# Optimization experiments

Hardware: AMD Instinct MI355X
Metric: run time of the kernel (lower is better)

The kernel has to match this reference:

```python
import jax, jax.numpy as jnp
import numpy as np

B, E, H, T = 32768, 64, 128, 12  # batch, embedding_dim, decoder_h_dim, pred_len


def setup_inputs() -> dict:
    key = jax.random.key(0)
    ks = jax.random.split(key, 13)
    f = lambda k, shape: jax.random.normal(k, shape, dtype=jnp.float32) * 0.05
    return {
        "last_pos": f(ks[0], (B, 2)),
        "last_pos_rel": f(ks[1], (B, 2)),
        "h0": f(ks[2], (1, B, H)),
        "c0": f(ks[3], (1, B, H)),
        "pred_ped_speed": jax.random.uniform(ks[4], (T, B, 1), dtype=jnp.float32),
        # spatial_embedding: Linear(3, E)
        "W_se": f(ks[5], (E, 3)),
        "b_se": f(ks[6], (E,)),
        # single-layer LSTM(E -> H), torch gate order [i, f, g, o]
        "W_ih": f(ks[7], (4 * H, E)),
        "W_hh": f(ks[8], (4 * H, H)),
        "b_ih": f(ks[9], (4 * H,)),
        "b_hh": f(ks[10], (4 * H,)),
        # hidden2pos: Linear(H, 2)
        "W_hp": f(ks[11], (2, H)),
        "b_hp": f(ks[12], (2,)),
    }


def reference(last_pos, last_pos_rel, h0, c0, pred_ped_speed,
              W_se, b_se, W_ih, W_hh, b_ih, b_hh, W_hp, b_hp):
    # train_or_test == 0 path: speed comes straight from pred_ped_speed
    Tlen = pred_ped_speed.shape[0]
    b_lstm = b_ih + b_hh
    # initial decoder input: embed concat([last_pos_rel, speed_0])  -> [B, E]
    x0 = jnp.concatenate([last_pos_rel, pred_ped_speed[0]], axis=1) @ W_se.T + b_se

    def step(carry, t):
        h, c, x, lp = carry  # h,c: [B,H]; x: [B,E]; lp: [B,2]
        gates = x @ W_ih.T + h @ W_hh.T + b_lstm           # [B, 4H]
        i, f_, g, o = jnp.split(gates, 4, axis=1)
        c = jax.nn.sigmoid(f_) * c + jax.nn.sigmoid(i) * jnp.tanh(g)
        h = jax.nn.sigmoid(o) * jnp.tanh(c)
        rel = h @ W_hp.T + b_hp                            # [B, 2]
        lp = rel + lp                                      # curr_pos -> last_pos
        # speed for next step; at final step torch keeps the previous speed
        spd = pred_ped_speed[jnp.minimum(t + 1, Tlen - 1)]
        x = jnp.concatenate([rel, spd], axis=1) @ W_se.T + b_se
        return (h, c, x, lp), rel

    (h, c, _, _), rels = jax.lax.scan(
        step, (h0[0], c0[0], x0, last_pos), jnp.arange(Tlen))
    # pred_traj_fake_rel: [T, B, 2]; final hidden state: [1, B, H]
    return rels, h[None]
```

## Files before the change

### kernel.cpp

```cpp
#include <hip/hip_runtime.h>

#define T_LEN 12
#define B_N   32768
#define H_N   128
#define BM    64

typedef __attribute__((ext_vector_type(8))) __bf16 bf16x8;
typedef __attribute__((ext_vector_type(8))) short  short8v;
typedef __attribute__((ext_vector_type(4))) float  f32x4;

__device__ __forceinline__ unsigned short f2bf(float f) {
  unsigned int u = __builtin_bit_cast(unsigned int, f);
  u += 0x7fffu + ((u >> 16) & 1u);
  return (unsigned short)(u >> 16);
}
__device__ __forceinline__ float sigm(float x) {
  return __builtin_amdgcn_rcpf(1.f + __builtin_amdgcn_exp2f(-1.4426950408889634f * x));
}
__device__ __forceinline__ float tanh_(float x) {
  return 1.f - 2.f * __builtin_amdgcn_rcpf(__builtin_amdgcn_exp2f(2.8853900817779268f * x) + 1.f);
}

__global__ void prep_kernel(const float* __restrict__ Wih, const float* __restrict__ Whh,
                            const float* __restrict__ bih, const float* __restrict__ bhh,
                            const float* __restrict__ Wse, const float* __restrict__ bse,
                            const float* __restrict__ Whp, const float* __restrict__ bhp,
                            unsigned short* __restrict__ WfReg, unsigned short* __restrict__ WfGO,
                            unsigned short* __restrict__ pBg, float* __restrict__ u,
                            float* __restrict__ w0, float* __restrict__ G) {
  int i = blockIdx.x * 256 + threadIdx.x;
  if (i < 65536) {
    int row = i >> 7, k = i & 127;
    float s = Whh[row * 128 + k];
    float wh0 = Whp[k], wh1 = Whp[128 + k];
    for (int e = 0; e < 64; ++e)
      s += Wih[row * 64 + e] * (Wse[e * 3 + 0] * wh0 + Wse[e * 3 + 1] * wh1);
    unsigned short v = f2bf(s);
    int g = row >> 7, unit = row & 127, w = unit >> 4, l15 = unit & 15;
    int ks = k >> 5, kg = (k >> 3) & 3, j = k & 7, l = kg * 16 + l15;
    if (g < 2) WfReg[((g * 4 + ks) * 512 + w * 64 + l) * 8 + j] = v;
    else       WfGO[(((g - 2) * 4 + ks) * 512 + w * 64 + l) * 8 + j] = v;
  } else if (i < 65536 + 2048) {
    int j = i - 65536;
    int n = j >> 2, which = j & 3;
    float s = 0.f;
    if (which < 2) {
      for (int e = 0; e < 64; ++e) s += Wih[n * 64 + e] * Wse[e * 3 + which];
      G[n * 2 + which] = s;
    } else if (which == 2) {
      for (int e = 0; e < 64; ++e) s += Wih[n * 64 + e] * Wse[e * 3 + 2];
      u[n] = s;
    } else {
      for (int e = 0; e < 64; ++e)
        s += Wih[n * 64 + e] * (bse[e] + Wse[e * 3 + 0] * bhp[0] + Wse[e * 3 + 1] * bhp[1]);
      w0[n] = bih[n] + bhh[n] + s;
    }
  } else if (i < 65536 + 2048 + 2048) {
    int idx = i - 65536 - 2048;
    int ks = idx >> 9, l = (idx >> 3) & 63, j = idx & 7;
    int c = l & 15, kg = l >> 4;
    pBg[idx] = (c < 2) ? f2bf(Whp[c * 128 + ks * 32 + kg * 8 + j]) : (unsigned short)0;
  }
}

__launch_bounds__(512, 2)
__global__ void decoder_kernel(const float* __restrict__ lpr,
                               const float* __restrict__ h0,
                               const float* __restrict__ c0,
                               const float* __restrict__ pps,
                               const float* __restrict__ Whp,
                               const float* __restrict__ bhp,
                               const unsigned short* __restrict__ WfReg,
                               const unsigned short* __restrict__ WfGO,
                               const unsigned short* __restrict__ pBg,
                               const float* __restrict__ u,
                               const float* __restrict__ w0,
                               const float* __restrict__ G,
                               float* __restrict__ out_rel,
                               float* __restrict__ out_h) {
  __shared__ unsigned short WgoL[32768];
  __shared__ unsigned short hA[2][BM * 128];
  __shared__ unsigned short pBL[2048];
  __shared__ float spdL[T_LEN * BM];
  __shared__ float dbuf[BM * 2];
  __shared__ float GL[1024];

  const int tid  = threadIdx.x;
  const int w    = tid >> 6;
  const int l    = tid & 63;
  const int l15  = l & 15;
  const int lg   = l >> 4;
  const int brow = blockIdx.x * BM;
  const int nh   = w * 16 + l15;
  const int swzA = (l15 & 7) << 4;

  short8v bw[2][4];
#pragma unroll
  for (int g = 0; g < 2; ++g)
#pragma unroll
    for (int ks = 0; ks < 4; ++ks)
      bw[g][ks] = *(const short8v*)(WfReg + ((g * 4 + ks) * 512 + tid) * 8);
#pragma unroll
  for (int it = 0; it < 8; ++it) {
    int idx = it * 512 + tid;
    *(short8v*)(WgoL + idx * 8) = *(const short8v*)(WfGO + idx * 8);
  }
  if (tid < 256) *(short8v*)(pBL + tid * 8) = *(const short8v*)(pBg + tid * 8);
  for (int i = tid; i < 1024; i += 512) GL[i] = G[i];
  for (int i = tid; i < T_LEN * BM; i += 512)
    spdL[i] = pps[(i >> 6) * B_N + brow + (i & 63)];

  float w0r[4], ur[4];
#pragma unroll
  for (int g = 0; g < 4; ++g) { w0r[g] = w0[g * 128 + nh]; ur[g] = u[g * 128 + nh]; }

  f32x4 cst[4];
#pragma unroll
  for (int rt = 0; rt < 4; ++rt)
#pragma unroll
    for (int r = 0; r < 4; ++r)
      cst[rt][r] = c0[(brow + rt * 16 + lg * 4 + r) * H_N + nh];

#pragma unroll
  for (int it = 0; it < 2; ++it) {
    int idx = it * 512 + tid;
    int row = idx >> 4, k0 = (idx & 15) * 8;
    const float* src = h0 + (brow + row) * H_N + k0;
    unsigned short tmp[8];
#pragma unroll
    for (int j = 0; j < 8; ++j) tmp[j] = f2bf(src[j]);
    *(short8v*)((char*)&hA[0][0] + ((row * 256 + k0 * 2) ^ ((row & 7) << 4))) = *(short8v*)tmp;
  }
  {
    int dot = tid >> 2, part = tid & 3;
    int row = dot >> 1, jj = dot & 1;
    float s = 0.f;
    const float* hrow = h0 + (brow + row) * H_N + part * 32;
    const float* wrow = Whp + jj * 128 + part * 32;
#pragma unroll
    for (int k = 0; k < 32; ++k) s += hrow[k] * wrow[k];
    s += __shfl_xor(s, 1); s += __shfl_xor(s, 2);
    if (part == 0) dbuf[dot] = lpr[(brow + row) * 2 + jj] - bhp[jj] - s;
  }
  const float bhpr = (l15 < 2) ? bhp[l15] : 0.f;

  char* rb = (char*)&hA[0][0];
  char* wbuf = (char*)&hA[1][0];

#pragma unroll 1
  for (int t = 0; t < T_LEN; ++t) {
    __syncthreads();
    f32x4 relC = (f32x4){0.f, 0.f, 0.f, 0.f};

#pragma unroll
    for (int rt = 0; rt < 4; ++rt) {
      f32x4 acc[4];
#pragma unroll
      for (int g = 0; g < 4; ++g) acc[g] = (f32x4){w0r[g], w0r[g], w0r[g], w0r[g]};

#pragma unroll
      for (int ks = 0; ks < 4; ++ks) {
        bf16x8 a = __builtin_bit_cast(bf16x8,
            *(short8v*)(rb + (((rt * 16 + l15) * 256 + ks * 64 + lg * 16) ^ swzA)));
        bf16x8 bg = __builtin_bit_cast(bf16x8, *(short8v*)(WgoL + (ks * 512 + tid) * 8));
        bf16x8 bo = __builtin_bit_cast(bf16x8, *(short8v*)(WgoL + ((4 + ks) * 512 + tid) * 8));
        acc[0] = __builtin_amdgcn_mfma_f32_16x16x32_bf16(a, __builtin_bit_cast(bf16x8, bw[0][ks]), acc[0], 0, 0, 0);
        acc[1] = __builtin_amdgcn_mfma_f32_16x16x32_bf16(a, __builtin_bit_cast(bf16x8, bw[1][ks]), acc[1], 0, 0, 0);
        acc[2] = __builtin_amdgcn_mfma_f32_16x16x32_bf16(a, bg, acc[2], 0, 0, 0);
        acc[3] = __builtin_amdgcn_mfma_f32_16x16x32_bf16(a, bo, acc[3], 0, 0, 0);
        if (w == rt && t > 0) {
          bf16x8 pb = __builtin_bit_cast(bf16x8, *(short8v*)(pBL + (ks * 64 + l) * 8));
          relC = __builtin_amdgcn_mfma_f32_16x16x32_bf16(a, pb, relC, 0, 0, 0);
        }
      }
      if (t == 0) {
#pragma unroll
        for (int r = 0; r < 4; ++r) {
          int row = rt * 16 + lg * 4 + r;
          float d0 = dbuf[row * 2 + 0], d1 = dbuf[row * 2 + 1];
#pragma unroll
          for (int g = 0; g < 4; ++g)
            acc[g][r] += d0 * GL[(g * 128 + nh) * 2 + 0] + d1 * GL[(g * 128 + nh) * 2 + 1];
        }
      }
#pragma unroll
      for (int r = 0; r < 4; ++r) {
        int row = rt * 16 + lg * 4 + r;
        float spd = spdL[t * BM + row];
        float gi = __builtin_fmaf(spd, ur[0], acc[0][r]);
        float gf = __builtin_fmaf(spd, ur[1], acc[1][r]);
        float gg = __builtin_fmaf(spd, ur[2], acc[2][r]);
        float go = __builtin_fmaf(spd, ur[3], acc[3][r]);
        float cn = sigm(gf) * cst[rt][r] + sigm(gi) * tanh_(gg);
        cst[rt][r] = cn;
        float h = sigm(go) * tanh_(cn);
        *(unsigned short*)(wbuf + ((row * 256 + nh * 2) ^ ((row & 7) << 4))) = f2bf(h);
        if (t == T_LEN - 1) out_h[(brow + row) * H_N + nh] = h;
      }
    }
    if (w < 4 && t > 0 && l15 < 2) {
#pragma unroll
      for (int r = 0; r < 4; ++r)
        out_rel[(size_t)(t - 1) * B_N * 2 + (brow + w * 16 + lg * 4 + r) * 2 + l15] = relC[r] + bhpr;
    }
    char* tmpp = rb; rb = wbuf; wbuf = tmpp;
  }

  __syncthreads();
  if (w < 4) {
    f32x4 relC = (f32x4){0.f, 0.f, 0.f, 0.f};
#pragma unroll
    for (int ks = 0; ks < 4; ++ks) {
      bf16x8 a = __builtin_bit_cast(bf16x8,
          *(short8v*)(rb + (((w * 16 + l15) * 256 + ks * 64 + lg * 16) ^ swzA)));
      bf16x8 pb = __builtin_bit_cast(bf16x8, *(short8v*)(pBL + (ks * 64 + l) * 8));
      relC = __builtin_amdgcn_mfma_f32_16x16x32_bf16(a, pb, relC, 0, 0, 0);
    }
    if (l15 < 2) {
#pragma unroll
      for (int r = 0; r < 4; ++r)
        out_rel[(size_t)(T_LEN - 1) * B_N * 2 + (brow + w * 16 + lg * 4 + r) * 2 + l15] = relC[r] + bhpr;
    }
  }
}

extern "C" void kernel_launch(void* const* d_in, const int* in_sizes, int n_in,
                              void* d_out, int out_size, void* d_ws, size_t ws_size,
                              hipStream_t stream) {
  const float* lpr  = (const float*)d_in[1];
  const float* h0   = (const float*)d_in[2];
  const float* c0   = (const float*)d_in[3];
  const float* pps  = (const float*)d_in[4];
  const float* W_se = (const float*)d_in[5];
  const float* b_se = (const float*)d_in[6];
  const float* W_ih = (const float*)d_in[7];
  const float* W_hh = (const float*)d_in[8];
  const float* b_ih = (const float*)d_in[9];
  const float* b_hh = (const float*)d_in[10];
  const float* W_hp = (const float*)d_in[11];
  const float* b_hp = (const float*)d_in[12];

  unsigned short* WfReg = (unsigned short*)d_ws;
  unsigned short* WfGO  = (unsigned short*)((char*)d_ws + 65536);
  unsigned short* pBg   = (unsigned short*)((char*)d_ws + 131072);
  float* u  = (float*)((char*)d_ws + 135168);
  float* w0 = (float*)((char*)d_ws + 137216);
  float* G  = (float*)((char*)d_ws + 139264);

  float* out_rel = (float*)d_out;
  float* out_h   = out_rel + (size_t)T_LEN * B_N * 2;

  hipLaunchKernelGGL(prep_kernel, dim3((65536 + 4096 + 255) / 256), dim3(256), 0, stream,
                     W_ih, W_hh, b_ih, b_hh, W_se, b_se, W_hp, b_hp,
                     WfReg, WfGO, pBg, u, w0, G);
  hipLaunchKernelGGL(decoder_kernel, dim3(B_N / BM), dim3(512), 0, stream,
                     lpr, h0, c0, pps, W_hp, b_hp, WfReg, WfGO, pBg, u, w0, G,
                     out_rel, out_h);
}
```

Measured before the change: 222.1 us.

## Double decoder block to 1024 threads, splitting batch rows across two wave groups

The decoder block grows from 8 to 16 waves. Each column wave-group now owns 32 of the 64 batch rows (2 row tiles instead of 4), which halves the serial MFMA and gate work per wave in each recurrent step. The per-column weight fragments are now duplicated in registers across both row groups, and setup loops are re-indexed for 1024 threads. The aim is better latency hiding and more concurrent waves per CU, since LDS use already limits residency to one block. The risk is that the aggressive launch bounds (1024, 4) cap registers and cause spills, and the wider block adds barrier cost.

```diff
diff --git a/kernel.cpp b/kernel.cpp
--- a/kernel.cpp
+++ b/kernel.cpp
@@ -63,7 +63,7 @@
   }
 }
 
-__launch_bounds__(512, 2)
+__launch_bounds__(1024, 4)
 __global__ void decoder_kernel(const float* __restrict__ lpr,
                                const float* __restrict__ h0,
                                const float* __restrict__ c0,
@@ -86,12 +86,15 @@
   __shared__ float GL[1024];
 
   const int tid  = threadIdx.x;
-  const int w    = tid >> 6;
+  const int wav  = tid >> 6;
+  const int wc   = wav & 7;
+  const int wr   = wav >> 3;
   const int l    = tid & 63;
   const int l15  = l & 15;
   const int lg   = l >> 4;
   const int brow = blockIdx.x * BM;
-  const int nh   = w * 16 + l15;
+  const int nh   = wc * 16 + l15;
+  const int rowb = wr * 32;
   const int swzA = (l15 & 7) << 4;
 
   short8v bw[2][4];
@@ -99,32 +102,29 @@
   for (int g = 0; g < 2; ++g)
 #pragma unroll
     for (int ks = 0; ks < 4; ++ks)
-      bw[g][ks] = *(const short8v*)(WfReg + ((g * 4 + ks) * 512 + tid) * 8);
-#pragma unroll
-  for (int it = 0; it < 8; ++it) {
-    int idx = it * 512 + tid;
+      bw[g][ks] = *(const short8v*)(WfReg + ((g * 4 + ks) * 512 + wc * 64 + l) * 8);
+#pragma unroll
+  for (int it = 0; it < 4; ++it) {
+    int idx = it * 1024 + tid;
     *(short8v*)(WgoL + idx * 8) = *(const short8v*)(WfGO + idx * 8);
   }
   if (tid < 256) *(short8v*)(pBL + tid * 8) = *(const short8v*)(pBg + tid * 8);
-  for (int i = tid; i < 1024; i += 512) GL[i] = G[i];
-  for (int i = tid; i < T_LEN * BM; i += 512)
-    spdL[i] = pps[(i >> 6) * B_N + brow + (i & 63)];
+  GL[tid & 1023] = G[tid & 1023];
+  if (tid < T_LEN * BM) spdL[tid] = pps[(tid >> 6) * B_N + brow + (tid & 63)];
 
   float w0r[4], ur[4];
 #pragma unroll
   for (int g = 0; g < 4; ++g) { w0r[g] = w0[g * 128 + nh]; ur[g] = u[g * 128 + nh]; }
 
-  f32x4 cst[4];
-#pragma unroll
-  for (int rt = 0; rt < 4; ++rt)
+  f32x4 cst[2];
+#pragma unroll
+  for (int rt = 0; rt < 2; ++rt)
 #pragma unroll
     for (int r = 0; r < 4; ++r)
-      cst[rt][r] = c0[(brow + rt * 16 + lg * 4 + r) * H_N + nh];
-
-#pragma unroll
-  for (int it = 0; it < 2; ++it) {
-    int idx = it * 512 + tid;
-    int row = idx >> 4, k0 = (idx & 15) * 8;
+      cst[rt][r] = c0[(brow + rowb + rt * 16 + lg * 4 + r) * H_N + nh];
+
+  {
+    int row = tid >> 4, k0 = (tid & 15) * 8;
     const float* src = h0 + (brow + row) * H_N + k0;
     unsigned short tmp[8];
 #pragma unroll
@@ -132,14 +132,14 @@
     *(short8v*)((char*)&hA[0][0] + ((row * 256 + k0 * 2) ^ ((row & 7) << 4))) = *(short8v*)tmp;
   }
   {
-    int dot = tid >> 2, part = tid & 3;
+    int dot = tid >> 3, part = tid & 7;
     int row = dot >> 1, jj = dot & 1;
     float s = 0.f;
-    const float* hrow = h0 + (brow + row) * H_N + part * 32;
-    const float* wrow = Whp + jj * 128 + part * 32;
-#pragma unroll
-    for (int k = 0; k < 32; ++k) s += hrow[k] * wrow[k];
-    s += __shfl_xor(s, 1); s += __shfl_xor(s, 2);
+    const float* hrow = h0 + (brow + row) * H_N + part * 16;
+    const float* wrow = Whp + jj * 128 + part * 16;
+#pragma unroll
+    for (int k = 0; k < 16; ++k) s += hrow[k] * wrow[k];
+    s += __shfl_xor(s, 1); s += __shfl_xor(s, 2); s += __shfl_xor(s, 4);
     if (part == 0) dbuf[dot] = lpr[(brow + row) * 2 + jj] - bhp[jj] - s;
   }
   const float bhpr = (l15 < 2) ? bhp[l15] : 0.f;
@@ -153,7 +153,7 @@
     f32x4 relC = (f32x4){0.f, 0.f, 0.f, 0.f};
 
 #pragma unroll
-    for (int rt = 0; rt < 4; ++rt) {
+    for (int rt = 0; rt < 2; ++rt) {
       f32x4 acc[4];
 #pragma unroll
       for (int g = 0; g < 4; ++g) acc[g] = (f32x4){w0r[g], w0r[g], w0r[g], w0r[g]};
@@ -161,14 +161,14 @@
 #pragma unroll
       for (int ks = 0; ks < 4; ++ks) {
         bf16x8 a = __builtin_bit_cast(bf16x8,
-            *(short8v*)(rb + (((rt * 16 + l15) * 256 + ks * 64 + lg * 16) ^ swzA)));
-        bf16x8 bg = __builtin_bit_cast(bf16x8, *(short8v*)(WgoL + (ks * 512 + tid) * 8));
-        bf16x8 bo = __builtin_bit_cast(bf16x8, *(short8v*)(WgoL + ((4 + ks) * 512 + tid) * 8));
+            *(short8v*)(rb + (((rowb + rt * 16 + l15) * 256 + ks * 64 + lg * 16) ^ swzA)));
+        bf16x8 bg = __builtin_bit_cast(bf16x8, *(short8v*)(WgoL + (ks * 512 + wc * 64 + l) * 8));
+        bf16x8 bo = __builtin_bit_cast(bf16x8, *(short8v*)(WgoL + ((4 + ks) * 512 + wc * 64 + l) * 8));
         acc[0] = __builtin_amdgcn_mfma_f32_16x16x32_bf16(a, __builtin_bit_cast(bf16x8, bw[0][ks]), acc[0], 0, 0, 0);
         acc[1] = __builtin_amdgcn_mfma_f32_16x16x32_bf16(a, __builtin_bit_cast(bf16x8, bw[1][ks]), acc[1], 0, 0, 0);
         acc[2] = __builtin_amdgcn_mfma_f32_16x16x32_bf16(a, bg, acc[2], 0, 0, 0);
         acc[3] = __builtin_amdgcn_mfma_f32_16x16x32_bf16(a, bo, acc[3], 0, 0, 0);
-        if (w == rt && t > 0) {
+        if (wc == rt && t > 0) {
           bf16x8 pb = __builtin_bit_cast(bf16x8, *(short8v*)(pBL + (ks * 64 + l) * 8));
           relC = __builtin_amdgcn_mfma_f32_16x16x32_bf16(a, pb, relC, 0, 0, 0);
         }
@@ -176,7 +176,7 @@
       if (t == 0) {
 #pragma unroll
         for (int r = 0; r < 4; ++r) {
-          int row = rt * 16 + lg * 4 + r;
+          int row = rowb + rt * 16 + lg * 4 + r;
           float d0 = dbuf[row * 2 + 0], d1 = dbuf[row * 2 + 1];
 #pragma unroll
           for (int g = 0; g < 4; ++g)
@@ -185,7 +185,7 @@
       }
 #pragma unroll
       for (int r = 0; r < 4; ++r) {
-        int row = rt * 16 + lg * 4 + r;
+        int row = rowb + rt * 16 + lg * 4 + r;
         float spd = spdL[t * BM + row];
         float gi = __builtin_fmaf(spd, ur[0], acc[0][r]);
         float gf = __builtin_fmaf(spd, ur[1], acc[1][r]);
@@ -198,28 +198,28 @@
         if (t == T_LEN - 1) out_h[(brow + row) * H_N + nh] = h;
       }
     }
-    if (w < 4 && t > 0 && l15 < 2) {
+    if (wc < 2 && t > 0 && l15 < 2) {
 #pragma unroll
       for (int r = 0; r < 4; ++r)
-        out_rel[(size_t)(t - 1) * B_N * 2 + (brow + w * 16 + lg * 4 + r) * 2 + l15] = relC[r] + bhpr;
+        out_rel[(size_t)(t - 1) * B_N * 2 + (brow + rowb + wc * 16 + lg * 4 + r) * 2 + l15] = relC[r] + bhpr;
     }
     char* tmpp = rb; rb = wbuf; wbuf = tmpp;
   }
 
   __syncthreads();
-  if (w < 4) {
+  if (wc < 2) {
     f32x4 relC = (f32x4){0.f, 0.f, 0.f, 0.f};
 #pragma unroll
     for (int ks = 0; ks < 4; ++ks) {
       bf16x8 a = __builtin_bit_cast(bf16x8,
-          *(short8v*)(rb + (((w * 16 + l15) * 256 + ks * 64 + lg * 16) ^ swzA)));
+          *(short8v*)(rb + (((rowb + wc * 16 + l15) * 256 + ks * 64 + lg * 16) ^ swzA)));
       bf16x8 pb = __builtin_bit_cast(bf16x8, *(short8v*)(pBL + (ks * 64 + l) * 8));
       relC = __builtin_amdgcn_mfma_f32_16x16x32_bf16(a, pb, relC, 0, 0, 0);
     }
     if (l15 < 2) {
 #pragma unroll
       for (int r = 0; r < 4; ++r)
-        out_rel[(size_t)(T_LEN - 1) * B_N * 2 + (brow + w * 16 + lg * 4 + r) * 2 + l15] = relC[r] + bhpr;
+        out_rel[(size_t)(T_LEN - 1) * B_N * 2 + (brow + rowb + wc * 16 + lg * 4 + r) * 2 + l15] = relC[r] + bhpr;
     }
   }
 }
@@ -253,7 +253,7 @@
   hipLaunchKernelGGL(prep_kernel, dim3((65536 + 4096 + 255) / 256), dim3(256), 0, stream,
                      W_ih, W_hh, b_ih, b_hh, W_se, b_se, W_hp, b_hp,
                      WfReg, WfGO, pBg, u, w0, G);
-  hipLaunchKernelGGL(decoder_kernel, dim3(B_N / BM), dim3(512), 0, stream,
+  hipLaunchKernelGGL(decoder_kernel, dim3(B_N / BM), dim3(1024), 0, stream,
                      lpr, h0, c0, pps, W_hp, b_hp, WfReg, WfGO, pBg, u, w0, G,
                      out_rel, out_h);
 }
```

New measurement: 231.6 us. 1.04x slower.
